# Performance work log

Hardware: AMD Instinct MI355X
Metric: run time of the kernel (lower is better)

## Reference

```python
import jax, jax.numpy as jnp
import numpy as np

N_NODES = 100000
N_EDGES = 1600000
IN_FEATS = 128
HIDDEN = 128
OUT_DIM = 128


def setup_inputs() -> dict:
    key = jax.random.key(0)
    ks = jax.random.split(key, 8)
    x = jax.random.normal(ks[0], (N_NODES, IN_FEATS), dtype=jnp.float32)
    W1 = jax.random.normal(ks[1], (IN_FEATS, HIDDEN), dtype=jnp.float32) * (1.0 / np.sqrt(IN_FEATS))
    b1 = jnp.zeros((HIDDEN,), dtype=jnp.float32)
    W2 = jax.random.normal(ks[2], (HIDDEN, HIDDEN), dtype=jnp.float32) * (1.0 / np.sqrt(HIDDEN))
    b2 = jnp.zeros((HIDDEN,), dtype=jnp.float32)
    W3 = jax.random.normal(ks[3], (HIDDEN, OUT_DIM), dtype=jnp.float32) * (1.0 / np.sqrt(HIDDEN))
    b3 = jnp.zeros((OUT_DIM,), dtype=jnp.float32)
    edge_src = jax.random.randint(ks[4], (N_EDGES,), 0, N_NODES, dtype=jnp.int32)
    edge_dst = jax.random.randint(ks[5], (N_EDGES,), 0, N_NODES, dtype=jnp.int32)
    return {"x": x, "W1": W1, "b1": b1, "W2": W2, "b2": b2, "W3": W3, "b3": b3,
            "edge_src": edge_src, "edge_dst": edge_dst}


def _mean_agg(h, edge_src, edge_dst, inv_deg):
    # gather src features, scatter-sum to dst, divide by in-degree (mean)
    summed = jax.ops.segment_sum(h[edge_src], edge_dst, num_segments=N_NODES)
    return summed * inv_deg[:, None]


def reference(x, W1, b1, W2, b2, W3, b3, edge_src, edge_dst):
    # in-degree (clamped to 1 to avoid div-by-zero, matching mean over empty = 0)
    deg = jax.ops.segment_sum(jnp.ones((N_EDGES,), dtype=jnp.float32), edge_dst,
                              num_segments=N_NODES)
    inv_deg = 1.0 / jnp.maximum(deg, 1.0)

    # DGL GINConv (eps=0, mean): h = Linear(h + mean_neighbors(h))
    h = x
    h = (h + _mean_agg(h, edge_src, edge_dst, inv_deg)) @ W1 + b1
    h = jax.nn.relu(h)  # dropout inactive in eval mode
    h = (h + _mean_agg(h, edge_src, edge_dst, inv_deg)) @ W2 + b2
    h = jax.nn.relu(h)
    h = (h + _mean_agg(h, edge_src, edge_dst, inv_deg)) @ W3 + b3
    return h
```

## Files before the change

### kernel.cpp

```cpp
#include <hip/hip_runtime.h>
#include <hip/hip_bf16.h>
#include <stdint.h>

#if __has_builtin(__builtin_amdgcn_cvt_pk_f32_fp8) && __has_builtin(__builtin_amdgcn_cvt_pk_fp8_f32)
#define FP8_HW 1
#else
#define FP8_HW 0
#include <hip/hip_fp8.h>
#endif

#define N_NODES 100000
#define N_EDGES 1600000
#define FEAT 128

#define BKT_SHIFT 8
#define BKT_SIZE  256
#define NB_BKT    391
#define BKT_CAP   5664
#define NB_SC     800
#define EPB_SC    2000

typedef uint16_t u16;
typedef uint32_t u32;
typedef __attribute__((ext_vector_type(8))) short bf16x8;
typedef __attribute__((ext_vector_type(4))) float f32x4;
typedef __attribute__((ext_vector_type(2))) float f32x2;

__device__ __forceinline__ u16 bf16_rn(float f){
  u32 u = __float_as_uint(f);
  u += 0x7FFFu + ((u >> 16) & 1u);
  return (u16)(u >> 16);
}
__device__ __forceinline__ float bf16_lo(u32 p){ return __uint_as_float(p << 16); }
__device__ __forceinline__ float bf16_hi(u32 p){ return __uint_as_float(p & 0xFFFF0000u); }

__device__ __forceinline__ void fp8x4_to_f32(u32 w, float* o){
#if FP8_HW
  f32x2 a = __builtin_amdgcn_cvt_pk_f32_fp8(w, false);
  f32x2 b = __builtin_amdgcn_cvt_pk_f32_fp8(w, true);
  o[0] = a.x; o[1] = a.y; o[2] = b.x; o[3] = b.y;
#else
  #pragma unroll
  for (int i = 0; i < 4; ++i){
    __hip_fp8_e4m3 t; t.__x = (uint8_t)((w >> (8 * i)) & 0xFF);
    o[i] = (float)t;
  }
#endif
}
__device__ __forceinline__ u32 f32x4_to_fp8(float a, float b, float c, float d){
#if FP8_HW
  u32 r = __builtin_amdgcn_cvt_pk_fp8_f32(a, b, 0, false);
  r = __builtin_amdgcn_cvt_pk_fp8_f32(c, d, r, true);
  return r;
#else
  __hip_fp8_e4m3 qa(a), qb(b), qc(c), qd(d);
  return (u32)qa.__x | ((u32)qb.__x << 8) | ((u32)qc.__x << 16) | ((u32)qd.__x << 24);
#endif
}


__global__ __launch_bounds__(512) void hist_kernel(const int* __restrict__ dst,
                                                   int* __restrict__ hcnt){
  __shared__ int h[NB_BKT];
  for (int i = threadIdx.x; i < NB_BKT; i += 512) h[i] = 0;
  __syncthreads();
  int base = blockIdx.x * EPB_SC;
  for (int e = base + threadIdx.x; e < base + EPB_SC; e += 512)
    atomicAdd(&h[dst[e] >> BKT_SHIFT], 1);
  __syncthreads();
  for (int i = threadIdx.x; i < NB_BKT; i += 512)
    hcnt[blockIdx.x * NB_BKT + i] = h[i];
}

__global__ void hscan_kernel(int* __restrict__ hcnt, int* __restrict__ cursor){
  __shared__ int s[256];
  int b = blockIdx.x, t = threadIdx.x;
  int v[4]; int sum = 0;
  #pragma unroll
  for (int j = 0; j < 4; ++j){
    int blk = 4 * t + j;
    v[j] = (blk < NB_SC) ? hcnt[blk * NB_BKT + b] : 0;
    sum += v[j];
  }
  s[t] = sum;
  __syncthreads();
  for (int d = 1; d < 256; d <<= 1){
    int add = (t >= d) ? s[t - d] : 0;
    __syncthreads();
    s[t] += add;
    __syncthreads();
  }
  int excl = s[t] - sum;
  #pragma unroll
  for (int j = 0; j < 4; ++j){
    int blk = 4 * t + j;
    if (blk < NB_SC){ hcnt[blk * NB_BKT + b] = excl; excl += v[j]; }
  }
  if (t == 255) cursor[b] = s[255];
}

__global__ __launch_bounds__(512) void scatter_kernel(const int* __restrict__ src,
                                                      const int* __restrict__ dst,
                                                      const int* __restrict__ hcnt,
                                                      uint2* __restrict__ bbuf){
  __shared__ int cur[NB_BKT];
  for (int i = threadIdx.x; i < NB_BKT; i += 512)
    cur[i] = hcnt[blockIdx.x * NB_BKT + i];
  __syncthreads();
  int base = blockIdx.x * EPB_SC;
  for (int e = base + threadIdx.x; e < base + EPB_SC; e += 512){
    int d = dst[e];
    int b = d >> BKT_SHIFT;
    int p = atomicAdd(&cur[b], 1);
    bbuf[(size_t)b * BKT_CAP + p] = make_uint2((u32)src[e], (u32)(d & (BKT_SIZE - 1)));
  }
}

__global__ __launch_bounds__(1024) void csr_build_kernel(const uint2* __restrict__ bbuf,
                                 const int* __restrict__ cursor,
                                 int* __restrict__ offs, int* __restrict__ deg,
                                 float* __restrict__ inv_deg, int* __restrict__ eidx){
  __shared__ int hist[BKT_SIZE];
  __shared__ int s[BKT_SIZE];
  __shared__ int cu[BKT_SIZE];
  int b = blockIdx.x;
  int t = threadIdx.x;
  int lo = b * BKT_CAP;
  int hi = lo + cursor[b];
  if (t < BKT_SIZE) hist[t] = 0;
  __syncthreads();
  for (int e = lo + t; e < hi; e += 1024)
    atomicAdd(&hist[bbuf[e].y], 1);
  __syncthreads();
  int v = 0, pv = 0;
  if (t < BKT_SIZE){
    v  = hist[t];
    pv = (v + 7) & ~7;
    s[t] = pv;
  }
  __syncthreads();
  for (int d = 1; d < BKT_SIZE; d <<= 1){
    int add = (t < BKT_SIZE && t >= d) ? s[t - d] : 0;
    __syncthreads();
    if (t < BKT_SIZE && t >= d) s[t] += add;
    __syncthreads();
  }
  if (t < BKT_SIZE){
    int excl = s[t] - pv;
    int node = b * BKT_SIZE + t;
    if (node < N_NODES){
      offs[node]    = lo + excl;
      deg[node]     = v;
      inv_deg[node] = 1.0f / fmaxf((float)v, 1.0f);
      for (int p = v; p < pv; ++p) eidx[lo + excl + p] = 0;
    }
    s[t]  = excl;
    cu[t] = 0;
  }
  __syncthreads();
  for (int e = lo + t; e < hi; e += 1024){
    uint2 q = bbuf[e];
    int p = atomicAdd(&cu[q.y], 1);
    eidx[lo + s[q.y] + p] = (int)q.x;
  }
}


__global__ void cvt_x8_kernel(const float* __restrict__ x, uint2* __restrict__ X8){
  int i = blockIdx.x * 256 + threadIdx.x;
  const float4* p = (const float4*)x + (size_t)i * 2;
  float4 a = p[0], b = p[1];
  uint2 o;
  o.x = f32x4_to_fp8(a.x, a.y, a.z, a.w);
  o.y = f32x4_to_fp8(b.x, b.y, b.z, b.w);
  X8[i] = o;
}

__global__ void wprep3_kernel(const float* __restrict__ W1, const float* __restrict__ W2,
                              const float* __restrict__ W3, u16* __restrict__ Wp1,
                              u16* __restrict__ Wp2, u16* __restrict__ Wp3){
  int which = blockIdx.x >> 6;
  int b     = blockIdx.x & 63;
  const float* W = (which == 0) ? W1 : (which == 1) ? W2 : W3;
  u16*        Wp = (which == 0) ? Wp1 : (which == 1) ? Wp2 : Wp3;
  int idx = b * 256 + threadIdx.x;
  int j    = idx & 7;
  int lane = (idx >> 3) & 63;
  int t    = idx >> 9;
  int k0 = t & 3, n0 = t >> 2;
  int k = k0 * 32 + (lane >> 4) * 8 + j;
  int n = n0 * 16 + (lane & 15);
  Wp[idx] = bf16_rn(W[k * FEAT + n]);
}


template<int SM, int OUT>
__global__ __launch_bounds__(64, 8) void layer_kernel(
    const u32* __restrict__ n8,
    const u16* __restrict__ hb,
    const float* __restrict__ xf,
    const int* __restrict__ offs,
    const int* __restrict__ deg,
    const float* __restrict__ inv_deg,
    const int* __restrict__ eidx,
    const u16* __restrict__ Wp,
    const float* __restrict__ bias,
    u16* __restrict__ Hout,
    u32* __restrict__ H8out,
    float* __restrict__ Fout){
  __shared__ u16 Tt[16 * FEAT];
  const int tid   = threadIdx.x;
  const int nsub  = tid >> 4;
  const int slice = tid & 15;
  const int base  = blockIdx.x * 16;

  for (int g = 0; g < 4; ++g){
    const int rrow = (g << 2) + nsub;
    const int node = base + rrow;
    const int start = offs[node];
    const int cnt   = deg[node];
    const int* ep = eidx + start;
    const int pcnt = (cnt + 7) & ~7;

    float acc[8];
    #pragma unroll
    for (int j = 0; j < 8; ++j) acc[j] = 0.f;

    uint4 qa = make_uint4(0,0,0,0), qb = qa;
    if (pcnt > 0){ qa = *(const uint4*)ep; qb = *(const uint4*)(ep + 4); }

    for (int e = 0; e < pcnt; e += 8){
      uint4 qa2 = *(const uint4*)(ep + e + 8);
      uint4 qb2 = *(const uint4*)(ep + e + 12);
      uint2 r0 = *(const uint2*)(n8 + (size_t)qa.x * 32 + slice * 2);
      uint2 r1 = *(const uint2*)(n8 + (size_t)qa.y * 32 + slice * 2);
      uint2 r2 = *(const uint2*)(n8 + (size_t)qa.z * 32 + slice * 2);
      uint2 r3 = *(const uint2*)(n8 + (size_t)qa.w * 32 + slice * 2);
      uint2 r4 = *(const uint2*)(n8 + (size_t)qb.x * 32 + slice * 2);
      uint2 r5 = *(const uint2*)(n8 + (size_t)qb.y * 32 + slice * 2);
      uint2 r6 = *(const uint2*)(n8 + (size_t)qb.z * 32 + slice * 2);
      uint2 r7 = *(const uint2*)(n8 + (size_t)qb.w * 32 + slice * 2);
      float t0[4], t1[4];
      #define ACC8(rr) \
        fp8x4_to_f32(rr.x, t0); fp8x4_to_f32(rr.y, t1); \
        acc[0]+=t0[0]; acc[1]+=t0[1]; acc[2]+=t0[2]; acc[3]+=t0[3]; \
        acc[4]+=t1[0]; acc[5]+=t1[1]; acc[6]+=t1[2]; acc[7]+=t1[3];
      ACC8(r0) ACC8(r1) ACC8(r2) ACC8(r3) ACC8(r4) ACC8(r5) ACC8(r6) ACC8(r7)
      #undef ACC8
      qa = qa2; qb = qb2;
    }

    if (pcnt > cnt){
      float f = (float)(pcnt - cnt);
      uint2 rz = *(const uint2*)(n8 + slice * 2);
      float t0[4], t1[4];
      fp8x4_to_f32(rz.x, t0); fp8x4_to_f32(rz.y, t1);
      acc[0]-=f*t0[0]; acc[1]-=f*t0[1]; acc[2]-=f*t0[2]; acc[3]-=f*t0[3];
      acc[4]-=f*t1[0]; acc[5]-=f*t1[1]; acc[6]-=f*t1[2]; acc[7]-=f*t1[3];
    }

    const float w = inv_deg[node];
    float self[8];
    if (SM == 1){
      const float* sp = xf + (size_t)node * FEAT + slice * 8;
      float4 a = *(const float4*)sp;
      float4 b = *(const float4*)(sp + 4);
      self[0]=a.x; self[1]=a.y; self[2]=a.z; self[3]=a.w;
      self[4]=b.x; self[5]=b.y; self[6]=b.z; self[7]=b.w;
    } else {
      const u16* sp = hb + (size_t)node * FEAT + slice * 8;
      uint4 s0 = *(const uint4*)sp;
      self[0]=bf16_lo(s0.x); self[1]=bf16_hi(s0.x); self[2]=bf16_lo(s0.y); self[3]=bf16_hi(s0.y);
      self[4]=bf16_lo(s0.z); self[5]=bf16_hi(s0.z); self[6]=bf16_lo(s0.w); self[7]=bf16_hi(s0.w);
    }
    uint4 o;
    o.x = (u32)bf16_rn(self[0] + w*acc[0]) | ((u32)bf16_rn(self[1] + w*acc[1]) << 16);
    o.y = (u32)bf16_rn(self[2] + w*acc[2]) | ((u32)bf16_rn(self[3] + w*acc[3]) << 16);
    o.z = (u32)bf16_rn(self[4] + w*acc[4]) | ((u32)bf16_rn(self[5] + w*acc[5]) << 16);
    o.w = (u32)bf16_rn(self[6] + w*acc[6]) | ((u32)bf16_rn(self[7] + w*acc[7]) << 16);
    ((uint4*)Tt)[rrow * 16 + (slice ^ (rrow & 7))] = o;
  }
  __syncthreads();

  const int quad = tid >> 4;
  const int c    = tid & 15;

  bf16x8 A[4];
  #pragma unroll
  for (int k0 = 0; k0 < 4; ++k0){
    uint4 t = ((const uint4*)Tt)[c * 16 + ((quad + k0 * 4) ^ (c & 7))];
    A[k0] = *(const bf16x8*)&t;
  }
  if (OUT == 0) __syncthreads();

  #pragma unroll
  for (int h = 0; h < 2; ++h){
    f32x4 acc2[4];
    #pragma unroll
    for (int i = 0; i < 4; ++i) acc2[i] = (f32x4){0.f, 0.f, 0.f, 0.f};
    #pragma unroll
    for (int i = 0; i < 4; ++i){
      int n0 = h * 4 + i;
      #pragma unroll
      for (int k0 = 0; k0 < 4; ++k0){
        bf16x8 b = *(const bf16x8*)(Wp + (size_t)(((n0 << 2) | k0) * 64 + tid) * 8);
        acc2[i] = __builtin_amdgcn_mfma_f32_16x16x32_bf16(A[k0], b, acc2[i], 0, 0, 0);
      }
    }
    #pragma unroll
    for (int i = 0; i < 4; ++i){
      int n0 = h * 4 + i;
      float bv = bias[n0 * 16 + c];
      #pragma unroll
      for (int r = 0; r < 4; ++r){
        int rr  = quad * 4 + r;
        int col = n0 * 16 + c;
        if (OUT == 1){
          Fout[(size_t)(base + rr) * FEAT + col] = acc2[i][r] + bv;
        } else {
          float v = fmaxf(acc2[i][r] + bv, 0.f);
          Tt[rr * FEAT + (col ^ ((rr & 7) << 3))] = bf16_rn(v);
        }
      }
    }
  }

  if (OUT == 0){
    __syncthreads();
    #pragma unroll
    for (int it = 0; it < 4; ++it){
      int p  = it * 64 + tid;
      int rr = p >> 4, qq = p & 15;
      int node = base + rr;
      uint4 d = ((const uint4*)Tt)[rr * 16 + (qq ^ (rr & 7))];
      *(uint4*)(Hout + (size_t)node * FEAT + qq * 8) = d;
      uint2 o8;
      o8.x = f32x4_to_fp8(bf16_lo(d.x), bf16_hi(d.x), bf16_lo(d.y), bf16_hi(d.y));
      o8.y = f32x4_to_fp8(bf16_lo(d.z), bf16_hi(d.z), bf16_lo(d.w), bf16_hi(d.w));
      *(uint2*)(H8out + (size_t)node * 32 + qq * 2) = o8;
    }
  }
}


static inline size_t align_up(size_t x){ return (x + 255) & ~(size_t)255; }

extern "C" void kernel_launch(void* const* d_in, const int* in_sizes, int n_in,
                              void* d_out, int out_size, void* d_ws, size_t ws_size,
                              hipStream_t stream){
  const float* x  = (const float*)d_in[0];
  const float* W1 = (const float*)d_in[1];
  const float* b1 = (const float*)d_in[2];
  const float* W2 = (const float*)d_in[3];
  const float* b2 = (const float*)d_in[4];
  const float* W3 = (const float*)d_in[5];
  const float* b3 = (const float*)d_in[6];
  const int* esrc = (const int*)d_in[7];
  const int* edst = (const int*)d_in[8];

  char* w = (char*)d_ws;
  int*   deg     = (int*)w;    w += align_up((size_t)N_NODES * 4);
  int*   offs    = (int*)w;    w += align_up((size_t)N_NODES * 4);
  float* inv_deg = (float*)w;  w += align_up((size_t)N_NODES * 4);
  int*   eidx    = (int*)w;    w += align_up((size_t)NB_BKT * BKT_CAP * 4);
  u16*   Wp1     = (u16*)w;    w += align_up((size_t)16384 * 2);
  u16*   Wp2     = (u16*)w;    w += align_up((size_t)16384 * 2);
  u16*   Wp3     = (u16*)w;    w += align_up((size_t)16384 * 2);
  u16*   Hb      = (u16*)w;    w += align_up((size_t)N_NODES * FEAT * 2);
  u32*   H8b     = (u32*)w;    w += align_up((size_t)N_NODES * 32 * 4);

  uint2* bbuf   = (uint2*)Hb;
  int*   cursor = (int*)H8b;
  int*   hcnt   = (int*)((char*)H8b + align_up((size_t)NB_BKT * 4));

  u16* Ha  = (u16*)d_out;
  u32* H8a = (u32*)((char*)d_out + (size_t)N_NODES * FEAT * 2);
  u32* X8  = (u32*)((char*)d_out + (size_t)N_NODES * FEAT * 3);

  hist_kernel<<<NB_SC, 512, 0, stream>>>(edst, hcnt);
  hscan_kernel<<<NB_BKT, 256, 0, stream>>>(hcnt, cursor);
  scatter_kernel<<<NB_SC, 512, 0, stream>>>(esrc, edst, hcnt, bbuf);
  csr_build_kernel<<<NB_BKT, 1024, 0, stream>>>(bbuf, cursor, offs, deg, inv_deg, eidx);

  wprep3_kernel<<<192, 256, 0, stream>>>(W1, W2, W3, Wp1, Wp2, Wp3);
  cvt_x8_kernel<<<N_EDGES / 256, 256, 0, stream>>>(x, (uint2*)X8);

  const int LAYER_BLOCKS = N_NODES / 16;

  layer_kernel<1, 0><<<LAYER_BLOCKS, 64, 0, stream>>>(
      X8, (const u16*)nullptr, x, offs, deg, inv_deg, eidx, Wp1, b1,
      Ha, H8a, (float*)nullptr);

  layer_kernel<0, 0><<<LAYER_BLOCKS, 64, 0, stream>>>(
      H8a, Ha, (const float*)nullptr, offs, deg, inv_deg, eidx, Wp2, b2,
      Hb, H8b, (float*)nullptr);

  layer_kernel<0, 1><<<LAYER_BLOCKS, 64, 0, stream>>>(
      H8b, Hb, (const float*)nullptr, offs, deg, inv_deg, eidx, Wp3, b3,
      (u16*)nullptr, (u32*)nullptr, (float*)d_out);

  (void)in_sizes; (void)n_in; (void)out_size; (void)ws_size; (void)w;
}
```

Before: 302.7 us.

## Replace bucketed CSR build with global atomics; widen layer blocks to two waves

Replaces the two-level bucket-sort CSR construction with a per-node degree count via global atomics, a block-partial scan and an atomic-cursor edge scatter into padded per-node slots. The layer kernel now uses 128 threads (two waves) per 16-node block, each wave aggregating 8 rows and computing half the output columns with MFMA. The gather loop is software-pipelined so the next 8 neighbor rows are fetched before the current ones are accumulated, using packed fp8 conversion. The intent is to cut CSR preprocessing cost and improve latency hiding in aggregation, at the cost of heavy global atomic contention and a nondeterministic edge order within each node.

```diff
diff --git a/kernel.cpp b/kernel.cpp
--- a/kernel.cpp
+++ b/kernel.cpp
@@ -12,13 +12,8 @@
 #define N_NODES 100000
 #define N_EDGES 1600000
 #define FEAT 128
-
-#define BKT_SHIFT 8
-#define BKT_SIZE  256
-#define NB_BKT    391
-#define BKT_CAP   5664
-#define NB_SC     800
-#define EPB_SC    2000
+#define NBLK_N 391
+#define EIDX_CAP 2400064
 
 typedef uint16_t u16;
 typedef uint32_t u32;
@@ -58,111 +53,95 @@
 #endif
 }
 
-
-__global__ __launch_bounds__(512) void hist_kernel(const int* __restrict__ dst,
-                                                   int* __restrict__ hcnt){
-  __shared__ int h[NB_BKT];
-  for (int i = threadIdx.x; i < NB_BKT; i += 512) h[i] = 0;
+__device__ __forceinline__ void acc_row(uint2 r, f32x2* acc){
+#if FP8_HW
+  acc[0] += __builtin_amdgcn_cvt_pk_f32_fp8(r.x, false);
+  acc[1] += __builtin_amdgcn_cvt_pk_f32_fp8(r.x, true);
+  acc[2] += __builtin_amdgcn_cvt_pk_f32_fp8(r.y, false);
+  acc[3] += __builtin_amdgcn_cvt_pk_f32_fp8(r.y, true);
+#else
+  float t0[4], t1[4];
+  fp8x4_to_f32(r.x, t0); fp8x4_to_f32(r.y, t1);
+  acc[0].x += t0[0]; acc[0].y += t0[1]; acc[1].x += t0[2]; acc[1].y += t0[3];
+  acc[2].x += t1[0]; acc[2].y += t1[1]; acc[3].x += t1[2]; acc[3].y += t1[3];
+#endif
+}
+
+
+__global__ __launch_bounds__(512) void zero_deg_kernel(int* __restrict__ deg){
+  int i = blockIdx.x * 512 + threadIdx.x;
+  if (i < N_NODES) deg[i] = 0;
+}
+
+__global__ __launch_bounds__(512) void degcnt_kernel(const int* __restrict__ dst,
+                                                     int* __restrict__ deg){
+  int e = blockIdx.x * 512 + threadIdx.x;
+  atomicAdd(&deg[dst[e]], 1);
+}
+
+__global__ __launch_bounds__(256) void degpart_kernel(const int* __restrict__ deg,
+                                                      int* __restrict__ part){
+  __shared__ int sred[4];
+  int i = blockIdx.x * 256 + threadIdx.x;
+  int d = (i < N_NODES) ? ((deg[i] + 7) & ~7) : 0;
+  #pragma unroll
+  for (int o = 32; o; o >>= 1) d += __shfl_xor(d, o);
+  int wv = threadIdx.x >> 6;
+  if ((threadIdx.x & 63) == 0) sred[wv] = d;
   __syncthreads();
-  int base = blockIdx.x * EPB_SC;
-  for (int e = base + threadIdx.x; e < base + EPB_SC; e += 512)
-    atomicAdd(&h[dst[e] >> BKT_SHIFT], 1);
+  if (threadIdx.x == 0) part[blockIdx.x] = sred[0] + sred[1] + sred[2] + sred[3];
+}
+
+__global__ __launch_bounds__(512) void scanp_kernel(int* __restrict__ part){
+  __shared__ int s[512];
+  int t = threadIdx.x;
+  int v = (t < NBLK_N) ? part[t] : 0;
+  s[t] = v;
   __syncthreads();
-  for (int i = threadIdx.x; i < NB_BKT; i += 512)
-    hcnt[blockIdx.x * NB_BKT + i] = h[i];
-}
-
-__global__ void hscan_kernel(int* __restrict__ hcnt, int* __restrict__ cursor){
+  for (int d = 1; d < 512; d <<= 1){
+    int add = (t >= d) ? s[t - d] : 0;
+    __syncthreads();
+    s[t] += add;
+    __syncthreads();
+  }
+  if (t < NBLK_N) part[t] = s[t] - v;
+}
+
+__global__ __launch_bounds__(256) void csr_offs_kernel(const int* __restrict__ deg,
+                               const int* __restrict__ part, int* __restrict__ offs,
+                               float* __restrict__ inv_deg, int* __restrict__ cursor,
+                               int* __restrict__ eidx){
   __shared__ int s[256];
   int b = blockIdx.x, t = threadIdx.x;
-  int v[4]; int sum = 0;
-  #pragma unroll
-  for (int j = 0; j < 4; ++j){
-    int blk = 4 * t + j;
-    v[j] = (blk < NB_SC) ? hcnt[blk * NB_BKT + b] : 0;
-    sum += v[j];
-  }
-  s[t] = sum;
+  int i = b * 256 + t;
+  int d  = (i < N_NODES) ? deg[i] : 0;
+  int pv = (d + 7) & ~7;
+  s[t] = pv;
   __syncthreads();
-  for (int d = 1; d < 256; d <<= 1){
-    int add = (t >= d) ? s[t - d] : 0;
+  for (int dd = 1; dd < 256; dd <<= 1){
+    int add = (t >= dd) ? s[t - dd] : 0;
     __syncthreads();
     s[t] += add;
     __syncthreads();
   }
-  int excl = s[t] - sum;
-  #pragma unroll
-  for (int j = 0; j < 4; ++j){
-    int blk = 4 * t + j;
-    if (blk < NB_SC){ hcnt[blk * NB_BKT + b] = excl; excl += v[j]; }
-  }
-  if (t == 255) cursor[b] = s[255];
-}
-
-__global__ __launch_bounds__(512) void scatter_kernel(const int* __restrict__ src,
-                                                      const int* __restrict__ dst,
-                                                      const int* __restrict__ hcnt,
-                                                      uint2* __restrict__ bbuf){
-  __shared__ int cur[NB_BKT];
-  for (int i = threadIdx.x; i < NB_BKT; i += 512)
-    cur[i] = hcnt[blockIdx.x * NB_BKT + i];
-  __syncthreads();
-  int base = blockIdx.x * EPB_SC;
-  for (int e = base + threadIdx.x; e < base + EPB_SC; e += 512){
-    int d = dst[e];
-    int b = d >> BKT_SHIFT;
-    int p = atomicAdd(&cur[b], 1);
-    bbuf[(size_t)b * BKT_CAP + p] = make_uint2((u32)src[e], (u32)(d & (BKT_SIZE - 1)));
-  }
-}
-
-__global__ __launch_bounds__(1024) void csr_build_kernel(const uint2* __restrict__ bbuf,
-                                 const int* __restrict__ cursor,
-                                 int* __restrict__ offs, int* __restrict__ deg,
-                                 float* __restrict__ inv_deg, int* __restrict__ eidx){
-  __shared__ int hist[BKT_SIZE];
-  __shared__ int s[BKT_SIZE];
-  __shared__ int cu[BKT_SIZE];
-  int b = blockIdx.x;
-  int t = threadIdx.x;
-  int lo = b * BKT_CAP;
-  int hi = lo + cursor[b];
-  if (t < BKT_SIZE) hist[t] = 0;
-  __syncthreads();
-  for (int e = lo + t; e < hi; e += 1024)
-    atomicAdd(&hist[bbuf[e].y], 1);
-  __syncthreads();
-  int v = 0, pv = 0;
-  if (t < BKT_SIZE){
-    v  = hist[t];
-    pv = (v + 7) & ~7;
-    s[t] = pv;
-  }
-  __syncthreads();
-  for (int d = 1; d < BKT_SIZE; d <<= 1){
-    int add = (t < BKT_SIZE && t >= d) ? s[t - d] : 0;
-    __syncthreads();
-    if (t < BKT_SIZE && t >= d) s[t] += add;
-    __syncthreads();
-  }
-  if (t < BKT_SIZE){
-    int excl = s[t] - pv;
-    int node = b * BKT_SIZE + t;
-    if (node < N_NODES){
-      offs[node]    = lo + excl;
-      deg[node]     = v;
-      inv_deg[node] = 1.0f / fmaxf((float)v, 1.0f);
-      for (int p = v; p < pv; ++p) eidx[lo + excl + p] = 0;
-    }
-    s[t]  = excl;
-    cu[t] = 0;
-  }
-  __syncthreads();
-  for (int e = lo + t; e < hi; e += 1024){
-    uint2 q = bbuf[e];
-    int p = atomicAdd(&cu[q.y], 1);
-    eidx[lo + s[q.y] + p] = (int)q.x;
-  }
+  if (i < N_NODES){
+    int o = part[b] + s[t] - pv;
+    offs[i]    = o;
+    inv_deg[i] = 1.0f / fmaxf((float)d, 1.0f);
+    cursor[i]  = 0;
+    for (int p = d; p < pv; ++p) eidx[o + p] = 0;
+    if (i == N_NODES - 1)
+      for (int p = pv; p < pv + 32; ++p) eidx[o + p] = 0;
+  }
+}
+
+__global__ __launch_bounds__(512) void escatter_kernel(const int* __restrict__ src,
+                               const int* __restrict__ dst, const int* __restrict__ offs,
+                               int* __restrict__ cursor, int* __restrict__ eidx){
+  int e = blockIdx.x * 512 + threadIdx.x;
+  int d = dst[e];
+  int p = atomicAdd(&cursor[d], 1);
+  eidx[offs[d] + p] = src[e];
 }
 
 
@@ -195,7 +174,7 @@
 
 
 template<int SM, int OUT>
-__global__ __launch_bounds__(64, 8) void layer_kernel(
+__global__ __launch_bounds__(128, 8) void layer_kernel(
     const u32* __restrict__ n8,
     const u16* __restrict__ hb,
     const float* __restrict__ xf,
@@ -210,53 +189,66 @@
     float* __restrict__ Fout){
   __shared__ u16 Tt[16 * FEAT];
   const int tid   = threadIdx.x;
-  const int nsub  = tid >> 4;
-  const int slice = tid & 15;
+  const int wid   = tid >> 6;
+  const int lane  = tid & 63;
+  const int nsub  = lane >> 4;
+  const int slice = lane & 15;
   const int base  = blockIdx.x * 16;
-
-  for (int g = 0; g < 4; ++g){
-    const int rrow = (g << 2) + nsub;
+  const u32* gbase = n8 + slice * 2;
+
+  for (int g = 0; g < 2; ++g){
+    const int rrow = wid * 8 + (g << 2) + nsub;
     const int node = base + rrow;
     const int start = offs[node];
     const int cnt   = deg[node];
+    const int pcnt  = (cnt + 7) & ~7;
     const int* ep = eidx + start;
-    const int pcnt = (cnt + 7) & ~7;
-
-    float acc[8];
+
+    f32x2 acc[4];
     #pragma unroll
-    for (int j = 0; j < 8; ++j) acc[j] = 0.f;
-
-    uint4 qa = make_uint4(0,0,0,0), qb = qa;
-    if (pcnt > 0){ qa = *(const uint4*)ep; qb = *(const uint4*)(ep + 4); }
+    for (int j = 0; j < 4; ++j) acc[j] = (f32x2){0.f, 0.f};
+
+    uint4 q0 = *(const uint4*)ep;
+    uint4 q1 = *(const uint4*)(ep + 4);
+    uint2 rc[8];
+    rc[0] = *(const uint2*)(gbase + (size_t)q0.x * 32);
+    rc[1] = *(const uint2*)(gbase + (size_t)q0.y * 32);
+    rc[2] = *(const uint2*)(gbase + (size_t)q0.z * 32);
+    rc[3] = *(const uint2*)(gbase + (size_t)q0.w * 32);
+    rc[4] = *(const uint2*)(gbase + (size_t)q1.x * 32);
+    rc[5] = *(const uint2*)(gbase + (size_t)q1.y * 32);
+    rc[6] = *(const uint2*)(gbase + (size_t)q1.z * 32);
+    rc[7] = *(const uint2*)(gbase + (size_t)q1.w * 32);
+    uint4 qn1 = *(const uint4*)(ep + 8);
+    uint4 qn2 = *(const uint4*)(ep + 12);
 
     for (int e = 0; e < pcnt; e += 8){
-      uint4 qa2 = *(const uint4*)(ep + e + 8);
-      uint4 qb2 = *(const uint4*)(ep + e + 12);
-      uint2 r0 = *(const uint2*)(n8 + (size_t)qa.x * 32 + slice * 2);
-      uint2 r1 = *(const uint2*)(n8 + (size_t)qa.y * 32 + slice * 2);
-      uint2 r2 = *(const uint2*)(n8 + (size_t)qa.z * 32 + slice * 2);
-      uint2 r3 = *(const uint2*)(n8 + (size_t)qa.w * 32 + slice * 2);
-      uint2 r4 = *(const uint2*)(n8 + (size_t)qb.x * 32 + slice * 2);
-      uint2 r5 = *(const uint2*)(n8 + (size_t)qb.y * 32 + slice * 2);
-      uint2 r6 = *(const uint2*)(n8 + (size_t)qb.z * 32 + slice * 2);
-      uint2 r7 = *(const uint2*)(n8 + (size_t)qb.w * 32 + slice * 2);
-      float t0[4], t1[4];
-      #define ACC8(rr) \
-        fp8x4_to_f32(rr.x, t0); fp8x4_to_f32(rr.y, t1); \
-        acc[0]+=t0[0]; acc[1]+=t0[1]; acc[2]+=t0[2]; acc[3]+=t0[3]; \
-        acc[4]+=t1[0]; acc[5]+=t1[1]; acc[6]+=t1[2]; acc[7]+=t1[3];
-      ACC8(r0) ACC8(r1) ACC8(r2) ACC8(r3) ACC8(r4) ACC8(r5) ACC8(r6) ACC8(r7)
-      #undef ACC8
-      qa = qa2; qb = qb2;
+      uint2 rn[8];
+      rn[0] = *(const uint2*)(gbase + (size_t)qn1.x * 32);
+      rn[1] = *(const uint2*)(gbase + (size_t)qn1.y * 32);
+      rn[2] = *(const uint2*)(gbase + (size_t)qn1.z * 32);
+      rn[3] = *(const uint2*)(gbase + (size_t)qn1.w * 32);
+      rn[4] = *(const uint2*)(gbase + (size_t)qn2.x * 32);
+      rn[5] = *(const uint2*)(gbase + (size_t)qn2.y * 32);
+      rn[6] = *(const uint2*)(gbase + (size_t)qn2.z * 32);
+      rn[7] = *(const uint2*)(gbase + (size_t)qn2.w * 32);
+      qn1 = *(const uint4*)(ep + e + 16);
+      qn2 = *(const uint4*)(ep + e + 20);
+      #pragma unroll
+      for (int j = 0; j < 8; ++j) acc_row(rc[j], acc);
+      #pragma unroll
+      for (int j = 0; j < 8; ++j) rc[j] = rn[j];
     }
 
     if (pcnt > cnt){
       float f = (float)(pcnt - cnt);
-      uint2 rz = *(const uint2*)(n8 + slice * 2);
-      float t0[4], t1[4];
-      fp8x4_to_f32(rz.x, t0); fp8x4_to_f32(rz.y, t1);
-      acc[0]-=f*t0[0]; acc[1]-=f*t0[1]; acc[2]-=f*t0[2]; acc[3]-=f*t0[3];
-      acc[4]-=f*t1[0]; acc[5]-=f*t1[1]; acc[6]-=f*t1[2]; acc[7]-=f*t1[3];
+      uint2 rz = *(const uint2*)gbase;
+      f32x2 z[4];
+      #pragma unroll
+      for (int j = 0; j < 4; ++j) z[j] = (f32x2){0.f, 0.f};
+      acc_row(rz, z);
+      #pragma unroll
+      for (int j = 0; j < 4; ++j) acc[j] -= f * z[j];
     }
 
     const float w = inv_deg[node];
@@ -274,16 +266,16 @@
       self[4]=bf16_lo(s0.z); self[5]=bf16_hi(s0.z); self[6]=bf16_lo(s0.w); self[7]=bf16_hi(s0.w);
     }
     uint4 o;
-    o.x = (u32)bf16_rn(self[0] + w*acc[0]) | ((u32)bf16_rn(self[1] + w*acc[1]) << 16);
-    o.y = (u32)bf16_rn(self[2] + w*acc[2]) | ((u32)bf16_rn(self[3] + w*acc[3]) << 16);
-    o.z = (u32)bf16_rn(self[4] + w*acc[4]) | ((u32)bf16_rn(self[5] + w*acc[5]) << 16);
-    o.w = (u32)bf16_rn(self[6] + w*acc[6]) | ((u32)bf16_rn(self[7] + w*acc[7]) << 16);
+    o.x = (u32)bf16_rn(self[0] + w*acc[0].x) | ((u32)bf16_rn(self[1] + w*acc[0].y) << 16);
+    o.y = (u32)bf16_rn(self[2] + w*acc[1].x) | ((u32)bf16_rn(self[3] + w*acc[1].y) << 16);
+    o.z = (u32)bf16_rn(self[4] + w*acc[2].x) | ((u32)bf16_rn(self[5] + w*acc[2].y) << 16);
+    o.w = (u32)bf16_rn(self[6] + w*acc[3].x) | ((u32)bf16_rn(self[7] + w*acc[3].y) << 16);
     ((uint4*)Tt)[rrow * 16 + (slice ^ (rrow & 7))] = o;
   }
   __syncthreads();
 
-  const int quad = tid >> 4;
-  const int c    = tid & 15;
+  const int quad = lane >> 4;
+  const int c    = lane & 15;
 
   bf16x8 A[4];
   #pragma unroll
@@ -293,43 +285,40 @@
   }
   if (OUT == 0) __syncthreads();
 
-  #pragma unroll
-  for (int h = 0; h < 2; ++h){
-    f32x4 acc2[4];
+  f32x4 acc2[4];
+  #pragma unroll
+  for (int i = 0; i < 4; ++i) acc2[i] = (f32x4){0.f, 0.f, 0.f, 0.f};
+  #pragma unroll
+  for (int i = 0; i < 4; ++i){
+    int n0 = wid * 4 + i;
     #pragma unroll
-    for (int i = 0; i < 4; ++i) acc2[i] = (f32x4){0.f, 0.f, 0.f, 0.f};
+    for (int k0 = 0; k0 < 4; ++k0){
+      bf16x8 b = *(const bf16x8*)(Wp + (size_t)(((n0 << 2) | k0) * 64 + lane) * 8);
+      acc2[i] = __builtin_amdgcn_mfma_f32_16x16x32_bf16(A[k0], b, acc2[i], 0, 0, 0);
+    }
+  }
+  #pragma unroll
+  for (int i = 0; i < 4; ++i){
+    int n0 = wid * 4 + i;
+    float bv = bias[n0 * 16 + c];
     #pragma unroll
-    for (int i = 0; i < 4; ++i){
-      int n0 = h * 4 + i;
-      #pragma unroll
-      for (int k0 = 0; k0 < 4; ++k0){
-        bf16x8 b = *(const bf16x8*)(Wp + (size_t)(((n0 << 2) | k0) * 64 + tid) * 8);
-        acc2[i] = __builtin_amdgcn_mfma_f32_16x16x32_bf16(A[k0], b, acc2[i], 0, 0, 0);
+    for (int r = 0; r < 4; ++r){
+      int rr  = quad * 4 + r;
+      int col = n0 * 16 + c;
+      if (OUT == 1){
+        Fout[(size_t)(base + rr) * FEAT + col] = acc2[i][r] + bv;
+      } else {
+        float v = fmaxf(acc2[i][r] + bv, 0.f);
+        Tt[rr * FEAT + (col ^ ((rr & 7) << 3))] = bf16_rn(v);
       }
     }
+  }
+
+  if (OUT == 0){
+    __syncthreads();
     #pragma unroll
-    for (int i = 0; i < 4; ++i){
-      int n0 = h * 4 + i;
-      float bv = bias[n0 * 16 + c];
-      #pragma unroll
-      for (int r = 0; r < 4; ++r){
-        int rr  = quad * 4 + r;
-        int col = n0 * 16 + c;
-        if (OUT == 1){
-          Fout[(size_t)(base + rr) * FEAT + col] = acc2[i][r] + bv;
-        } else {
-          float v = fmaxf(acc2[i][r] + bv, 0.f);
-          Tt[rr * FEAT + (col ^ ((rr & 7) << 3))] = bf16_rn(v);
-        }
-      }
-    }
-  }
-
-  if (OUT == 0){
-    __syncthreads();
-    #pragma unroll
-    for (int it = 0; it < 4; ++it){
-      int p  = it * 64 + tid;
+    for (int it = 0; it < 2; ++it){
+      int p  = it * 128 + tid;
       int rr = p >> 4, qq = p & 15;
       int node = base + rr;
       uint4 d = ((const uint4*)Tt)[rr * 16 + (qq ^ (rr & 7))];
@@ -362,40 +351,40 @@
   int*   deg     = (int*)w;    w += align_up((size_t)N_NODES * 4);
   int*   offs    = (int*)w;    w += align_up((size_t)N_NODES * 4);
   float* inv_deg = (float*)w;  w += align_up((size_t)N_NODES * 4);
-  int*   eidx    = (int*)w;    w += align_up((size_t)NB_BKT * BKT_CAP * 4);
+  int*   cursor  = (int*)w;    w += align_up((size_t)N_NODES * 4);
+  int*   part    = (int*)w;    w += align_up((size_t)NBLK_N * 4);
+  int*   eidx    = (int*)w;    w += align_up((size_t)EIDX_CAP * 4);
   u16*   Wp1     = (u16*)w;    w += align_up((size_t)16384 * 2);
   u16*   Wp2     = (u16*)w;    w += align_up((size_t)16384 * 2);
   u16*   Wp3     = (u16*)w;    w += align_up((size_t)16384 * 2);
   u16*   Hb      = (u16*)w;    w += align_up((size_t)N_NODES * FEAT * 2);
   u32*   H8b     = (u32*)w;    w += align_up((size_t)N_NODES * 32 * 4);
 
-  uint2* bbuf   = (uint2*)Hb;
-  int*   cursor = (int*)H8b;
-  int*   hcnt   = (int*)((char*)H8b + align_up((size_t)NB_BKT * 4));
-
   u16* Ha  = (u16*)d_out;
   u32* H8a = (u32*)((char*)d_out + (size_t)N_NODES * FEAT * 2);
   u32* X8  = (u32*)((char*)d_out + (size_t)N_NODES * FEAT * 3);
 
-  hist_kernel<<<NB_SC, 512, 0, stream>>>(edst, hcnt);
-  hscan_kernel<<<NB_BKT, 256, 0, stream>>>(hcnt, cursor);
-  scatter_kernel<<<NB_SC, 512, 0, stream>>>(esrc, edst, hcnt, bbuf);
-  csr_build_kernel<<<NB_BKT, 1024, 0, stream>>>(bbuf, cursor, offs, deg, inv_deg, eidx);
+  zero_deg_kernel<<<(N_NODES + 511) / 512, 512, 0, stream>>>(deg);
+  degcnt_kernel<<<N_EDGES / 512, 512, 0, stream>>>(edst, deg);
+  degpart_kernel<<<NBLK_N, 256, 0, stream>>>(deg, part);
+  scanp_kernel<<<1, 512, 0, stream>>>(part);
+  csr_offs_kernel<<<NBLK_N, 256, 0, stream>>>(deg, part, offs, inv_deg, cursor, eidx);
+  escatter_kernel<<<N_EDGES / 512, 512, 0, stream>>>(esrc, edst, offs, cursor, eidx);
 
   wprep3_kernel<<<192, 256, 0, stream>>>(W1, W2, W3, Wp1, Wp2, Wp3);
   cvt_x8_kernel<<<N_EDGES / 256, 256, 0, stream>>>(x, (uint2*)X8);
 
   const int LAYER_BLOCKS = N_NODES / 16;
 
-  layer_kernel<1, 0><<<LAYER_BLOCKS, 64, 0, stream>>>(
+  layer_kernel<1, 0><<<LAYER_BLOCKS, 128, 0, stream>>>(
       X8, (const u16*)nullptr, x, offs, deg, inv_deg, eidx, Wp1, b1,
       Ha, H8a, (float*)nullptr);
 
-  layer_kernel<0, 0><<<LAYER_BLOCKS, 64, 0, stream>>>(
+  layer_kernel<0, 0><<<LAYER_BLOCKS, 128, 0, stream>>>(
       H8a, Ha, (const float*)nullptr, offs, deg, inv_deg, eidx, Wp2, b2,
       Hb, H8b, (float*)nullptr);
 
-  layer_kernel<0, 1><<<LAYER_BLOCKS, 64, 0, stream>>>(
+  layer_kernel<0, 1><<<LAYER_BLOCKS, 128, 0, stream>>>(
       H8b, Hb, (const float*)nullptr, offs, deg, inv_deg, eidx, Wp3, b3,
       (u16*)nullptr, (u32*)nullptr, (float*)d_out);
 
```

New measurement: 433.4 us. +43.2%, slower.
